# Performance work log

Hardware: AMD Instinct MI355X
Metric: run time of the kernel (lower is better)

Reference implementation:

```python
import math
import jax, jax.numpy as jnp
import numpy as np

B, SQ, SKV = 4, 2048, 2048
D_EMBED, D_CROSS, D_ATT, N_HEADS = 1024, 768, 1024, 16
D_HEAD = D_ATT // N_HEADS


def setup_inputs() -> dict:
    key = jax.random.key(0)
    ks = jax.random.split(key, 10)
    s_e = 1.0 / math.sqrt(D_EMBED)
    s_c = 1.0 / math.sqrt(D_CROSS)
    s_a = 1.0 / math.sqrt(D_ATT)
    return {
        "x": jax.random.normal(ks[0], (B, SQ, D_EMBED), jnp.float32),
        "y": jax.random.normal(ks[1], (B, SKV, D_CROSS), jnp.float32),
        "Wq": jax.random.normal(ks[2], (D_EMBED, D_ATT), jnp.float32) * s_e,
        "bq": jax.random.normal(ks[3], (D_ATT,), jnp.float32) * 0.01,
        "Wk": jax.random.normal(ks[4], (D_CROSS, D_ATT), jnp.float32) * s_c,
        "bk": jax.random.normal(ks[5], (D_ATT,), jnp.float32) * 0.01,
        "Wv": jax.random.normal(ks[6], (D_CROSS, D_ATT), jnp.float32) * s_c,
        "bv": jax.random.normal(ks[7], (D_ATT,), jnp.float32) * 0.01,
        "Wo": jax.random.normal(ks[8], (D_ATT, D_EMBED), jnp.float32) * s_a,
        "bo": jax.random.normal(ks[9], (D_EMBED,), jnp.float32) * 0.01,
    }


def _split_heads(t):
    b, s, _ = t.shape
    return t.reshape(b, s, N_HEADS, D_HEAD).transpose(0, 2, 1, 3)  # (b,h,s,dh)


def reference(x, y, Wq, bq, Wk, bk, Wv, bv, Wo, bo):
    q = _split_heads(x @ Wq + bq)   # (b,h,sq,dh)
    k = _split_heads(y @ Wk + bk)   # (b,h,skv,dh)
    v = _split_heads(y @ Wv + bv)   # (b,h,skv,dh)
    scale = 1.0 / math.sqrt(D_HEAD)
    scores = jnp.einsum('bhqd,bhkd->bhqk', q, k) * scale
    weights = jax.nn.softmax(scores, axis=-1)
    out = jnp.einsum('bhqk,bhkd->bhqd', weights, v)
    out = out.transpose(0, 2, 1, 3).reshape(x.shape[0], x.shape[1], D_ATT)
    return out @ Wo + bo
```

## Files before the change

### kernel.cpp

```cpp
#include <hip/hip_runtime.h>

typedef unsigned short u16;
typedef __attribute__((ext_vector_type(8))) short bf16x8;
typedef __attribute__((ext_vector_type(4))) float f32x4;

#define B_N 4
#define SQ 2048
#define SKV 2048
#define DE 1024
#define DC 768
#define DA 1024
#define NH 16
#define DH 64
#define MTOT (B_N * SQ)

__device__ __forceinline__ u16 f2bf(float f) {
    unsigned u = __float_as_uint(f);
    u += 0x7FFF + ((u >> 16) & 1);
    return (u16)(u >> 16);
}
__device__ __forceinline__ f32x4 mfma_bf16(bf16x8 a, bf16x8 b, f32x4 c) {
    return __builtin_amdgcn_mfma_f32_16x16x32_bf16(a, b, c, 0, 0, 0);
}
__device__ __forceinline__ void gload16(const void* g, void* l) {
    __builtin_amdgcn_global_load_lds(
        (const __attribute__((address_space(1))) unsigned int*)g,
        (__attribute__((address_space(3))) unsigned int*)l, 16, 0, 0);
}
__device__ __forceinline__ unsigned cvtpk(float a, float b) {
    unsigned r;
    asm("v_cvt_pk_bf16_f32 %0, %1, %2" : "=v"(r) : "v"(a), "v"(b));
    return r;
}

__global__ __launch_bounds__(256) void k_cvt(const float* __restrict__ s, u16* __restrict__ d) {
    size_t i = ((size_t)blockIdx.x * 256 + threadIdx.x) * 8;
    float4 v0 = *(const float4*)(s + i);
    float4 v1 = *(const float4*)(s + i + 4);
    uint4 u;
    u.x = cvtpk(v0.x, v0.y);
    u.y = cvtpk(v0.z, v0.w);
    u.z = cvtpk(v1.x, v1.y);
    u.w = cvtpk(v1.z, v1.w);
    *(uint4*)(d + i) = u;
}

__global__ __launch_bounds__(256) void k_tsplit(const float* __restrict__ W,
                                                u16* __restrict__ Th,
                                                int K, int N, float scale) {
    __shared__ float t[32][33];
    const int k0 = blockIdx.x * 32, n0 = blockIdx.y * 32;
    const int tx = threadIdx.x & 31, ty = threadIdx.x >> 5;
#pragma unroll
    for (int i = 0; i < 4; ++i)
        t[ty + 8 * i][tx] = W[(size_t)(k0 + ty + 8 * i) * N + (n0 + tx)];
    __syncthreads();
#pragma unroll
    for (int i = 0; i < 4; ++i) {
        float v = t[tx][ty + 8 * i] * scale;
        Th[(size_t)(n0 + ty + 8 * i) * K + (k0 + tx)] = f2bf(v);
    }
}

template <int KTOT, int EPI>
__global__ __launch_bounds__(256) void k_gemm(const u16* __restrict__ Ab,
                                              const u16* __restrict__ Bb,
                                              const float* __restrict__ bias,
                                              float bscale,
                                              float* __restrict__ C,
                                              u16* __restrict__ Cb) {
    __shared__ u16 sA[128 * 64], sB[128 * 64];
    const int tid = threadIdx.x;
    const int lane = tid & 63, w = tid >> 6;
    const int wm = w >> 1, wn = w & 1;
    const int g = lane >> 4, r16 = lane & 15;
    const int m0 = blockIdx.x * 128, n0 = blockIdx.y * 128;
    const int xa = r16 & 7;

    const f32x4 fzero = {0.f, 0.f, 0.f, 0.f};
    f32x4 acc[4][4];
#pragma unroll
    for (int i = 0; i < 4; ++i)
#pragma unroll
        for (int j = 0; j < 4; ++j) acc[i][j] = fzero;

    for (int kt = 0; kt < KTOT / 64; ++kt) {
#pragma unroll
        for (int i = 0; i < 4; ++i) {
            int slot = tid + i * 256;
            int row = slot >> 3, cs = slot & 7;
            size_t off = (size_t)(m0 + row) * (KTOT * 2) + (size_t)kt * 128 +
                         (size_t)((cs ^ (row & 7)) << 4);
            gload16((const char*)Ab + off, (char*)sA + slot * 16);
            size_t boff = (size_t)(n0 + row) * (KTOT * 2) + (size_t)kt * 128 +
                          (size_t)((cs ^ (row & 7)) << 4);
            gload16((const char*)Bb + boff, (char*)sB + slot * 16);
        }
        __syncthreads();
        bf16x8 ah[4][2], bh[4][2];
#pragma unroll
        for (int f = 0; f < 4; ++f)
#pragma unroll
            for (int s = 0; s < 2; ++s) {
                const int ar = wm * 64 + f * 16 + r16;
                const int br = wn * 64 + f * 16 + r16;
                const int cb = ((s * 4 + g) ^ xa) << 4;
                ah[f][s] = *(const bf16x8*)((const char*)sA + ar * 128 + cb);
                bh[f][s] = *(const bf16x8*)((const char*)sB + br * 128 + cb);
            }
        __builtin_amdgcn_s_setprio(1);
#pragma unroll
        for (int s = 0; s < 2; ++s)
#pragma unroll
            for (int fm = 0; fm < 4; ++fm)
#pragma unroll
                for (int fn = 0; fn < 4; ++fn)
                    acc[fm][fn] = mfma_bf16(ah[fm][s], bh[fn][s], acc[fm][fn]);
        __builtin_amdgcn_s_setprio(0);
        __syncthreads();
    }

#pragma unroll
    for (int fn = 0; fn < 4; ++fn) {
        const int col = n0 + wn * 64 + fn * 16 + r16;
        const float bv = bias[col] * bscale;
        const int h = col >> 6, dh = col & 63;
#pragma unroll
        for (int fm = 0; fm < 4; ++fm)
#pragma unroll
            for (int r = 0; r < 4; ++r) {
                const int row = m0 + wm * 64 + fm * 16 + g * 4 + r;
                const float v = acc[fm][fn][r] + bv;
                if constexpr (EPI == 0) {
                    C[(size_t)row * 1024 + col] = v;
                } else if constexpr (EPI == 3) {
                    Cb[(size_t)row * 1024 + col] = f2bf(v);
                } else {
                    const int b = row >> 11, kv = row & 2047;
                    const int t = kv >> 6, kvr = kv & 63;
                    const size_t tb = (size_t)((b * 16 + h) * 32 + t) * 8192;
                    if constexpr (EPI == 1) {
                        const int drow = (kvr & 3) * 16 + (kvr >> 2);
                        Cb[tb + drow * 64 + (((dh >> 3) ^ (drow & 7)) << 3) + (dh & 7)] = f2bf(v);
                    } else {
                        Cb[tb + 4096 + dh * 64 + (((kvr >> 3) ^ (dh & 7)) << 3) + (kvr & 7)] = f2bf(v);
                    }
                }
            }
    }
}

__global__ __launch_bounds__(256, 2) void k_attn(const u16* __restrict__ Qb,
                                                 const u16* __restrict__ KV,
                                                 u16* __restrict__ Af) {
    __shared__ u16 sKV[2][8192];
    __shared__ u16 Ps[4][64][64];
    const int lin = blockIdx.x;
    const int swz = (lin & 7) * 64 + (lin >> 3);
    const int qt = swz & 7, bh = swz >> 3;
    const int b = bh >> 4, h = bh & 15;
    const int tid = threadIdx.x, lane = tid & 63, w = tid >> 6;
    const int g = lane >> 4, r16 = lane & 15;
    const int xk = (r16 & 7) << 4;
    const int qbase = qt * 256 + w * 64;

    bf16x8 qh[4][2];
#pragma unroll
    for (int rf = 0; rf < 4; ++rf) {
        const size_t qrow = (size_t)(b * SQ + qbase + rf * 16 + r16);
#pragma unroll
        for (int s = 0; s < 2; ++s)
            qh[rf][s] = *(const bf16x8*)&Qb[qrow * DA + h * 64 + s * 32 + g * 8];
    }

    const f32x4 fzero = {0.f, 0.f, 0.f, 0.f};
    f32x4 oacc[4][4];
    f32x4 l_run[4];
#pragma unroll
    for (int rf = 0; rf < 4; ++rf) {
        l_run[rf] = fzero;
#pragma unroll
        for (int i = 0; i < 4; ++i) oacc[rf][i] = fzero;
    }

    char* pw = (char*)&Ps[w][0][0];
    const char* gb0 = (const char*)KV + (size_t)bh * 32 * 16384;

#pragma unroll
    for (int i = 0; i < 4; ++i) {
        int c = w * 4 + i;
        gload16(gb0 + c * 1024 + lane * 16, (char*)&sKV[0][0] + c * 1024);
    }

    for (int t = 0; t < SKV / 64; ++t) {
        const int cur = t & 1;
        __syncthreads();
        {
            const char* gnext = gb0 + (size_t)((t + 1) & 31) * 16384;
            char* lnext = (char*)&sKV[cur ^ 1][0];
#pragma unroll
            for (int i = 0; i < 4; ++i) {
                int c = w * 4 + i;
                gload16(gnext + c * 1024 + lane * 16, lnext + c * 1024);
            }
        }
        const char* smb = (const char*)&sKV[cur][0];

        bf16x8 kh[4][2];
#pragma unroll
        for (int f = 0; f < 4; ++f)
#pragma unroll
            for (int s = 0; s < 2; ++s)
                kh[f][s] = *(const bf16x8*)(smb + (f * 16 + r16) * 128 + ((s * 64 + g * 16) ^ xk));

#pragma unroll
        for (int rf = 0; rf < 4; ++rf) {
            f32x4 sacc[4];
#pragma unroll
            for (int f = 0; f < 4; ++f) sacc[f] = fzero;
            __builtin_amdgcn_s_setprio(1);
#pragma unroll
            for (int f = 0; f < 4; ++f)
#pragma unroll
                for (int s = 0; s < 2; ++s)
                    sacc[f] = mfma_bf16(qh[rf][s], kh[f][s], sacc[f]);
            __builtin_amdgcn_s_setprio(0);
#pragma unroll
            for (int r = 0; r < 4; ++r) {
                float p0 = __expf(sacc[0][r]);
                float p1 = __expf(sacc[1][r]);
                float p2 = __expf(sacc[2][r]);
                float p3 = __expf(sacc[3][r]);
                l_run[rf][r] += (p0 + p1) + (p2 + p3);
                int prow = rf * 16 + g * 4 + r;
                uint2 pk;
                pk.x = cvtpk(p0, p1);
                pk.y = cvtpk(p2, p3);
                *(uint2*)(pw + prow * 128 + ((r16 * 8) ^ ((prow & 7) << 4))) = pk;
            }
        }

        bf16x8 pa[4][2];
#pragma unroll
        for (int rf = 0; rf < 4; ++rf)
#pragma unroll
            for (int s = 0; s < 2; ++s)
                pa[rf][s] = *(const bf16x8*)(pw + (rf * 16 + r16) * 128 + ((s * 64 + g * 16) ^ xk));
#pragma unroll
        for (int fd = 0; fd < 4; ++fd)
#pragma unroll
            for (int s = 0; s < 2; ++s) {
                bf16x8 vh = *(const bf16x8*)(smb + 8192 + (fd * 16 + r16) * 128 + ((s * 64 + g * 16) ^ xk));
                __builtin_amdgcn_s_setprio(1);
#pragma unroll
                for (int rf = 0; rf < 4; ++rf)
                    oacc[rf][fd] = mfma_bf16(pa[rf][s], vh, oacc[rf][fd]);
                __builtin_amdgcn_s_setprio(0);
            }
    }

#pragma unroll
    for (int rf = 0; rf < 4; ++rf)
#pragma unroll
        for (int x = 1; x < 16; x <<= 1)
#pragma unroll
            for (int r = 0; r < 4; ++r) l_run[rf][r] += __shfl_xor(l_run[rf][r], x);

#pragma unroll
    for (int rf = 0; rf < 4; ++rf) {
        float linv[4];
#pragma unroll
        for (int r = 0; r < 4; ++r) linv[r] = 1.0f / l_run[rf][r];
#pragma unroll
        for (int fd = 0; fd < 4; ++fd)
#pragma unroll
            for (int r = 0; r < 4; ++r) {
                int row = qbase + rf * 16 + g * 4 + r;
                Af[(size_t)(b * SQ + row) * DA + h * 64 + fd * 16 + r16] =
                    f2bf(oacc[rf][fd][r] * linv[r]);
            }
    }
}

extern "C" void kernel_launch(void* const* d_in, const int* in_sizes, int n_in,
                              void* d_out, int out_size, void* d_ws, size_t ws_size,
                              hipStream_t stream) {
    const float* x = (const float*)d_in[0];
    const float* y = (const float*)d_in[1];
    const float* Wq = (const float*)d_in[2];
    const float* bq = (const float*)d_in[3];
    const float* Wk = (const float*)d_in[4];
    const float* bk = (const float*)d_in[5];
    const float* Wv = (const float*)d_in[6];
    const float* bv = (const float*)d_in[7];
    const float* Wo = (const float*)d_in[8];
    const float* bo = (const float*)d_in[9];
    float* out = (float*)d_out;

    char* p = (char*)d_ws;
    u16* Qb = (u16*)p; p += (size_t)MTOT * DA * 2;
    u16* Af = (u16*)p; p += (size_t)MTOT * DA * 2;
    u16* xb = (u16*)p; p += (size_t)MTOT * DE * 2;
    u16* yb = (u16*)p; p += (size_t)MTOT * DC * 2;
    u16* KV = (u16*)p; p += (size_t)64 * 32 * 8192 * 2;
    u16* wq = (u16*)p; p += (size_t)DE * DA * 2;
    u16* wk = (u16*)p; p += (size_t)DC * DA * 2;
    u16* wv = (u16*)p; p += (size_t)DC * DA * 2;
    u16* wo = (u16*)p; p += (size_t)DA * DE * 2;

    k_cvt<<<MTOT * DE / 2048, 256, 0, stream>>>(x, xb);
    k_cvt<<<MTOT * DC / 2048, 256, 0, stream>>>(y, yb);

    k_tsplit<<<dim3(DE / 32, DA / 32), 256, 0, stream>>>(Wq, wq, DE, DA, 0.125f);
    k_tsplit<<<dim3(DC / 32, DA / 32), 256, 0, stream>>>(Wk, wk, DC, DA, 1.0f);
    k_tsplit<<<dim3(DC / 32, DA / 32), 256, 0, stream>>>(Wv, wv, DC, DA, 1.0f);
    k_tsplit<<<dim3(DA / 32, DE / 32), 256, 0, stream>>>(Wo, wo, DA, DE, 1.0f);

    k_gemm<DE, 3><<<dim3(MTOT / 128, DA / 128), 256, 0, stream>>>(xb, wq, bq, 0.125f, nullptr, Qb);
    k_gemm<DC, 1><<<dim3(MTOT / 128, DA / 128), 256, 0, stream>>>(yb, wk, bk, 1.0f, nullptr, KV);
    k_gemm<DC, 2><<<dim3(MTOT / 128, DA / 128), 256, 0, stream>>>(yb, wv, bv, 1.0f, nullptr, KV);

    k_attn<<<dim3(512), 256, 0, stream>>>(Qb, KV, Af);

    k_gemm<DA, 0><<<dim3(MTOT / 128, DE / 128), 256, 0, stream>>>(Af, wo, bo, 1.0f, out, nullptr);
}
```

Before: 192.7 us.

## Double-buffer GEMM LDS tiles and fold log2e into Q scale for exp2

The GEMM kernel now uses two LDS buffers for A and B. It prefetches the next K tile while computing on the current one, which drops one barrier per iteration and overlaps global loads with MFMA work. Separately, the Q projection scale now includes log2(e), so the attention softmax can use exp2f in place of __expf. Doubling the LDS footprint to 64KB per block may reduce occupancy.

```diff
diff --git a/kernel.cpp b/kernel.cpp
--- a/kernel.cpp
+++ b/kernel.cpp
@@ -13,6 +13,7 @@
 #define NH 16
 #define DH 64
 #define MTOT (B_N * SQ)
+#define LOG2E 1.44269504088896f
 
 __device__ __forceinline__ u16 f2bf(float f) {
     unsigned u = __float_as_uint(f);
@@ -69,13 +70,14 @@
                                               float bscale,
                                               float* __restrict__ C,
                                               u16* __restrict__ Cb) {
-    __shared__ u16 sA[128 * 64], sB[128 * 64];
+    __shared__ u16 sA[2][128 * 64], sB[2][128 * 64];
     const int tid = threadIdx.x;
     const int lane = tid & 63, w = tid >> 6;
     const int wm = w >> 1, wn = w & 1;
     const int g = lane >> 4, r16 = lane & 15;
     const int m0 = blockIdx.x * 128, n0 = blockIdx.y * 128;
     const int xa = r16 & 7;
+    const int NT = KTOT / 64;
 
     const f32x4 fzero = {0.f, 0.f, 0.f, 0.f};
     f32x4 acc[4][4];
@@ -84,19 +86,34 @@
 #pragma unroll
         for (int j = 0; j < 4; ++j) acc[i][j] = fzero;
 
-    for (int kt = 0; kt < KTOT / 64; ++kt) {
-#pragma unroll
-        for (int i = 0; i < 4; ++i) {
-            int slot = tid + i * 256;
-            int row = slot >> 3, cs = slot & 7;
-            size_t off = (size_t)(m0 + row) * (KTOT * 2) + (size_t)kt * 128 +
-                         (size_t)((cs ^ (row & 7)) << 4);
-            gload16((const char*)Ab + off, (char*)sA + slot * 16);
-            size_t boff = (size_t)(n0 + row) * (KTOT * 2) + (size_t)kt * 128 +
-                          (size_t)((cs ^ (row & 7)) << 4);
-            gload16((const char*)Bb + boff, (char*)sB + slot * 16);
+#pragma unroll
+    for (int i = 0; i < 4; ++i) {
+        int slot = tid + i * 256;
+        int row = slot >> 3, cs = slot & 7;
+        size_t off = (size_t)(m0 + row) * (KTOT * 2) + (size_t)((cs ^ (row & 7)) << 4);
+        gload16((const char*)Ab + off, (char*)&sA[0][0] + slot * 16);
+        size_t boff = (size_t)(n0 + row) * (KTOT * 2) + (size_t)((cs ^ (row & 7)) << 4);
+        gload16((const char*)Bb + boff, (char*)&sB[0][0] + slot * 16);
+    }
+
+    for (int kt = 0; kt < NT; ++kt) {
+        const int cur = kt & 1;
+        __syncthreads();
+        if (kt + 1 < NT) {
+#pragma unroll
+            for (int i = 0; i < 4; ++i) {
+                int slot = tid + i * 256;
+                int row = slot >> 3, cs = slot & 7;
+                size_t off = (size_t)(m0 + row) * (KTOT * 2) + (size_t)(kt + 1) * 128 +
+                             (size_t)((cs ^ (row & 7)) << 4);
+                gload16((const char*)Ab + off, (char*)&sA[cur ^ 1][0] + slot * 16);
+                size_t boff = (size_t)(n0 + row) * (KTOT * 2) + (size_t)(kt + 1) * 128 +
+                              (size_t)((cs ^ (row & 7)) << 4);
+                gload16((const char*)Bb + boff, (char*)&sB[cur ^ 1][0] + slot * 16);
+            }
         }
-        __syncthreads();
+        const char* pA = (const char*)&sA[cur][0];
+        const char* pB = (const char*)&sB[cur][0];
         bf16x8 ah[4][2], bh[4][2];
 #pragma unroll
         for (int f = 0; f < 4; ++f)
@@ -105,8 +122,8 @@
                 const int ar = wm * 64 + f * 16 + r16;
                 const int br = wn * 64 + f * 16 + r16;
                 const int cb = ((s * 4 + g) ^ xa) << 4;
-                ah[f][s] = *(const bf16x8*)((const char*)sA + ar * 128 + cb);
-                bh[f][s] = *(const bf16x8*)((const char*)sB + br * 128 + cb);
+                ah[f][s] = *(const bf16x8*)(pA + ar * 128 + cb);
+                bh[f][s] = *(const bf16x8*)(pB + br * 128 + cb);
             }
         __builtin_amdgcn_s_setprio(1);
 #pragma unroll
@@ -117,7 +134,6 @@
                 for (int fn = 0; fn < 4; ++fn)
                     acc[fm][fn] = mfma_bf16(ah[fm][s], bh[fn][s], acc[fm][fn]);
         __builtin_amdgcn_s_setprio(0);
-        __syncthreads();
     }
 
 #pragma unroll
@@ -227,10 +243,10 @@
             __builtin_amdgcn_s_setprio(0);
 #pragma unroll
             for (int r = 0; r < 4; ++r) {
-                float p0 = __expf(sacc[0][r]);
-                float p1 = __expf(sacc[1][r]);
-                float p2 = __expf(sacc[2][r]);
-                float p3 = __expf(sacc[3][r]);
+                float p0 = exp2f(sacc[0][r]);
+                float p1 = exp2f(sacc[1][r]);
+                float p2 = exp2f(sacc[2][r]);
+                float p3 = exp2f(sacc[3][r]);
                 l_run[rf][r] += (p0 + p1) + (p2 + p3);
                 int prow = rf * 16 + g * 4 + r;
                 uint2 pk;
@@ -308,15 +324,17 @@
     u16* wv = (u16*)p; p += (size_t)DC * DA * 2;
     u16* wo = (u16*)p; p += (size_t)DA * DE * 2;
 
+    const float qs = 0.125f * LOG2E;
+
     k_cvt<<<MTOT * DE / 2048, 256, 0, stream>>>(x, xb);
     k_cvt<<<MTOT * DC / 2048, 256, 0, stream>>>(y, yb);
 
-    k_tsplit<<<dim3(DE / 32, DA / 32), 256, 0, stream>>>(Wq, wq, DE, DA, 0.125f);
+    k_tsplit<<<dim3(DE / 32, DA / 32), 256, 0, stream>>>(Wq, wq, DE, DA, qs);
     k_tsplit<<<dim3(DC / 32, DA / 32), 256, 0, stream>>>(Wk, wk, DC, DA, 1.0f);
     k_tsplit<<<dim3(DC / 32, DA / 32), 256, 0, stream>>>(Wv, wv, DC, DA, 1.0f);
     k_tsplit<<<dim3(DA / 32, DE / 32), 256, 0, stream>>>(Wo, wo, DA, DE, 1.0f);
 
-    k_gemm<DE, 3><<<dim3(MTOT / 128, DA / 128), 256, 0, stream>>>(xb, wq, bq, 0.125f, nullptr, Qb);
+    k_gemm<DE, 3><<<dim3(MTOT / 128, DA / 128), 256, 0, stream>>>(xb, wq, bq, qs, nullptr, Qb);
     k_gemm<DC, 1><<<dim3(MTOT / 128, DA / 128), 256, 0, stream>>>(yb, wk, bk, 1.0f, nullptr, KV);
     k_gemm<DC, 2><<<dim3(MTOT / 128, DA / 128), 256, 0, stream>>>(yb, wv, bv, 1.0f, nullptr, KV);
 
```

Result: slower. 221.1 us (+14.7%).
